# Optimization experiments

Measured on AMD Instinct MI355X. Metric: run time of the kernel, lower is better.

## Reference

```python
import jax, jax.numpy as jnp
import numpy as np

N, E, IN_FEATS, HID, HEADS = 50000, 800000, 256, 32, 8
NEG_SLOPE = 0.2


def _init_params(key):
    ks = jax.random.split(key, 12)
    def lin(k, fi, fo):
        return jax.random.normal(k, (fi, fo), jnp.float32) * (1.0 / np.sqrt(fi))
    p = {}
    # layer 0: in_feats -> HID x HEADS
    p['W0'] = lin(ks[0], IN_FEATS, HEADS * HID)
    p['al0'] = jax.random.normal(ks[1], (HEADS, HID), jnp.float32) * 0.1
    p['ar0'] = jax.random.normal(ks[2], (HEADS, HID), jnp.float32) * 0.1
    p['b0'] = jnp.zeros((HEADS * HID,), jnp.float32)
    # layer 1: HID*HEADS -> HID x HEADS
    p['W1'] = lin(ks[3], HEADS * HID, HEADS * HID)
    p['al1'] = jax.random.normal(ks[4], (HEADS, HID), jnp.float32) * 0.1
    p['ar1'] = jax.random.normal(ks[5], (HEADS, HID), jnp.float32) * 0.1
    p['b1'] = jnp.zeros((HEADS * HID,), jnp.float32)
    # layer 2 (final): HID*HEADS -> HID x 1 head, no activation
    p['W2'] = lin(ks[6], HEADS * HID, HID)
    p['al2'] = jax.random.normal(ks[7], (1, HID), jnp.float32) * 0.1
    p['ar2'] = jax.random.normal(ks[8], (1, HID), jnp.float32) * 0.1
    p['b2'] = jnp.zeros((HID,), jnp.float32)
    return p


def setup_inputs() -> dict:
    key = jax.random.key(0)
    k1, k2, k3, kp = jax.random.split(key, 4)
    inp = {
        'features': jax.random.normal(k1, (N, IN_FEATS), jnp.float32),
        'src': jax.random.randint(k2, (E,), 0, N, jnp.int32),
        'dst': jax.random.randint(k3, (E,), 0, N, jnp.int32),
    }
    inp.update(_init_params(kp))
    return inp


def _gat_layer(x, src, dst, W, al, ar, b, heads, act):
    n = x.shape[0]
    d = W.shape[1] // heads
    feat = (x @ W).reshape(n, heads, d)           # [N,H,D]
    el = jnp.sum(feat * al, axis=-1)              # [N,H]
    er = jnp.sum(feat * ar, axis=-1)              # [N,H]
    e = jax.nn.leaky_relu(el[src] + er[dst], NEG_SLOPE)   # [E,H]
    # segment softmax over destination neighborhoods
    emax = jax.ops.segment_max(e, dst, num_segments=n)
    ex = jnp.exp(e - emax[dst])
    denom = jax.ops.segment_sum(ex, dst, num_segments=n)
    a = ex / (denom[dst] + 1e-9)                  # [E,H]
    msg = feat[src] * a[:, :, None]               # [E,H,D]
    out = jax.ops.segment_sum(msg, dst, num_segments=n)   # [N,H,D]
    out = out + b.reshape(1, heads, d)
    return act(out) if act is not None else out


def reference(features, src, dst, W0, al0, ar0, b0, W1, al1, ar1, b1, W2, al2, ar2, b2):
    h = _gat_layer(features, src, dst, W0, al0, ar0, b0, HEADS, jax.nn.elu)
    h = h.reshape(h.shape[0], -1)
    h = _gat_layer(h, src, dst, W1, al1, ar1, b1, HEADS, jax.nn.elu)
    h = h.reshape(h.shape[0], -1)
    h = _gat_layer(h, src, dst, W2, al2, ar2, b2, 1, None)   # [N,1,D]
    return h.mean(axis=1)                                    # [N,D]
```

## Files before the change

kernel.cpp:

```cpp
#include <hip/hip_runtime.h>

typedef unsigned short u16;
typedef unsigned int   u32;
typedef __attribute__((ext_vector_type(8))) short  short8;
typedef __attribute__((ext_vector_type(4))) float  f32x4;
typedef __attribute__((ext_vector_type(2))) float  f32x2;
typedef __attribute__((ext_vector_type(2))) unsigned int u32v2;
typedef __attribute__((ext_vector_type(4))) unsigned int u32v4;

#define NN 50000
#define NE 800000

__device__ __forceinline__ float bf2f(u16 b) { return __uint_as_float(((u32)b) << 16); }
__device__ __forceinline__ float bflo(u32 p) { return __uint_as_float(p << 16); }
__device__ __forceinline__ float bfhi(u32 p) { return __uint_as_float(p & 0xffff0000u); }
__device__ __forceinline__ u16 f2bf(float f) {
    u32 u = __float_as_uint(f);
    u32 r = u + 0x7fffu + ((u >> 16) & 1u);
    return (u16)(r >> 16);
}
__device__ __forceinline__ float lexp(float v) {
    v = fmaxf(v, 0.2f * v);
    return __expf(fminf(v, 60.f));
}

__device__ __forceinline__ int block_detect(const u32* x, int n, int* sh, int* sz) {
    int t = threadIdx.x;
    int hits = 0, nz = 0;
    for (int i = t; i < n; i += 256) {
        u32 w = x[i];
        if (w) {
            ++nz;
            u32 e = (w >> 7) & 0xffu;
            if (e >= 100 && e <= 150) ++hits;
        }
    }
    sh[t] = hits; sz[t] = nz;
    __syncthreads();
    for (int ofs = 128; ofs > 0; ofs >>= 1) {
        if (t < ofs) { sh[t] += sh[t + ofs]; sz[t] += sz[t + ofs]; }
        __syncthreads();
    }
    return (sz[0] == 0) ? 2 : ((sh[0] * 2 >= sz[0]) ? 0 : 1);
}

struct PrepArgs {
    const u32* dp[13]; int dnw[13];
    const void* cs[9]; float* cd[9]; int cn[9];
    const void* wsrc[3]; u16* wdst[3]; int wN[3]; int wchunks[3];
    int* deg; int degn;
};

__global__ __launch_bounds__(256) void k_prep(PrepArgs a, int* flags) {
    __shared__ int sh[256], sz[256];
    const int bid = blockIdx.x;
    const int t = threadIdx.x;
    if (bid < 13) {
        int f = block_detect(a.dp[bid], a.dnw[bid], sh, sz);
        if (t == 0) flags[bid] = f;
    } else if (bid < 22) {
        const int j = bid - 13;
        int nw = a.cn[j] / 2; if (nw > 512) nw = 512;
        const int fl = block_detect((const u32*)a.cs[j], nw, sh, sz);
        if (t < a.cn[j]) {
            float v = 0.f;
            if (fl == 1) v = ((const float*)a.cs[j])[t];
            else if (fl == 0) v = bf2f(((const u16*)a.cs[j])[t]);
            a.cd[j][t] = v;
        }
    } else if (bid < 90) {
        int wj, base;
        if (bid < 54)      { wj = 0; base = 22; }
        else if (bid < 86) { wj = 1; base = 54; }
        else               { wj = 2; base = 86; }
        const void* Wsrc = a.wsrc[wj];
        const int fl = block_detect((const u32*)Wsrc, 512, sh, sz);
        const int id = (bid - base) * 256 + t;
        if (id < a.wchunks[wj]) {
            const int L = id & 63, kt = (id >> 6) & 7, nt = id >> 9;
            const int col = nt * 16 + (L & 15);
            const int krow = kt * 32 + ((L >> 4) & 3) * 8;
            const bool isf32 = (fl == 1);
            const int N = a.wN[wj];
            u16* Wp = a.wdst[wj];
#pragma unroll
            for (int j2 = 0; j2 < 8; ++j2) {
                int s = (krow + j2) * N + col;
                Wp[id * 8 + j2] = isf32 ? f2bf(((const float*)Wsrc)[s])
                                        : ((const u16*)Wsrc)[s];
            }
        }
    } else {
        const int i = (bid - 90) * 256 + t;
        if (i < a.degn) a.deg[i] = 0;
    }
}

__global__ void k_hist(const int* __restrict__ dst, int* __restrict__ deg, int E) {
    int e = blockIdx.x * 256 + threadIdx.x;
    if (e < E) atomicAdd(&deg[dst[e]], 1);
}

__global__ __launch_bounds__(256) void k_scan_partial(const int* __restrict__ deg,
                                                      int* __restrict__ bsum, int n) {
    __shared__ int red[256];
    int t = threadIdx.x;
    int i = blockIdx.x * 256 + t;
    red[t] = (i < n) ? deg[i] : 0;
    __syncthreads();
    for (int ofs = 128; ofs > 0; ofs >>= 1) {
        if (t < ofs) red[t] += red[t + ofs];
        __syncthreads();
    }
    if (t == 0) bsum[blockIdx.x] = red[0];
}

__global__ __launch_bounds__(256) void k_scan_bsum(int* __restrict__ bsum, int nb) {
    __shared__ int s[256];
    int t = threadIdx.x;
    int v = (t < nb) ? bsum[t] : 0;
    s[t] = v;
    __syncthreads();
    for (int ofs = 1; ofs < 256; ofs <<= 1) {
        int x = (t >= ofs) ? s[t - ofs] : 0;
        __syncthreads();
        s[t] += x;
        __syncthreads();
    }
    if (t < nb) bsum[t] = s[t] - v;
}

__global__ __launch_bounds__(256) void k_scan_final(const int* __restrict__ deg,
                                                    const int* __restrict__ bsum,
                                                    int* __restrict__ rowptr,
                                                    int* __restrict__ cursor, int n) {
    __shared__ int s[256];
    int t = threadIdx.x;
    int i = blockIdx.x * 256 + t;
    int v = (i < n) ? deg[i] : 0;
    s[t] = v;
    __syncthreads();
    for (int ofs = 1; ofs < 256; ofs <<= 1) {
        int x = (t >= ofs) ? s[t - ofs] : 0;
        __syncthreads();
        s[t] += x;
        __syncthreads();
    }
    int excl = bsum[blockIdx.x] + s[t] - v;
    if (i < n) {
        rowptr[i] = excl;
        cursor[i] = excl;
        if (i == n - 1) rowptr[n] = excl + v;
    }
}

__global__ void k_scatter(const int* __restrict__ src, const int* __restrict__ dst,
                          int* __restrict__ cursor, int* __restrict__ csr_src, int E) {
    int e = blockIdx.x * 256 + threadIdx.x;
    if (e >= E) return;
    int p = atomicAdd(&cursor[dst[e]], 1);
    csr_src[p] = src[e];
}

__global__ __launch_bounds__(512) void k_gemm_mfma(const void* __restrict__ Xv,
                                                   const int* __restrict__ xflag,
                                                   const u16* __restrict__ Wp,
                                                   u16* __restrict__ OUT, int nrows) {
    __shared__ u16 As[64 * 256];
    const int t = threadIdx.x;
    const int w = t >> 6, L = t & 63;
    const int quad = (L >> 4) & 3;
    const int r0 = blockIdx.x * 64;
    const bool xf32 = (xflag != nullptr) && (*xflag == 1);

    short8* Asv = (short8*)As;
    short8 zero = {0, 0, 0, 0, 0, 0, 0, 0};
#pragma unroll
    for (int i = 0; i < 4; ++i) {
        int g = i * 512 + t;
        int row = g >> 5, cc = g & 31;
        int r = r0 + row;
        short8 val = zero;
        if (r < nrows) {
            if (xf32) {
                const f32x4* Xf4 = (const f32x4*)Xv;
                f32x4 lo = Xf4[(size_t)r * 64 + cc * 2];
                f32x4 hi = Xf4[(size_t)r * 64 + cc * 2 + 1];
                val[0] = (short)f2bf(lo[0]); val[1] = (short)f2bf(lo[1]);
                val[2] = (short)f2bf(lo[2]); val[3] = (short)f2bf(lo[3]);
                val[4] = (short)f2bf(hi[0]); val[5] = (short)f2bf(hi[1]);
                val[6] = (short)f2bf(hi[2]); val[7] = (short)f2bf(hi[3]);
            } else {
                val = ((const short8*)Xv)[(size_t)r * 32 + cc];
            }
        }
        Asv[cc * 64 + (row ^ (cc & 7))] = val;
    }

    const short8* Wv = (const short8*)Wp;
    short8 bf[2][8];
#pragma unroll
    for (int jn = 0; jn < 2; ++jn) {
        int nt = w + jn * 8;
#pragma unroll
        for (int kt = 0; kt < 8; ++kt) bf[jn][kt] = Wv[(nt * 8 + kt) * 64 + L];
    }
    __syncthreads();

    f32x4 acc[4][2];
#pragma unroll
    for (int mi = 0; mi < 4; ++mi)
#pragma unroll
        for (int jn = 0; jn < 2; ++jn) acc[mi][jn] = (f32x4){0.f, 0.f, 0.f, 0.f};

#pragma unroll
    for (int kt = 0; kt < 8; ++kt) {
        const int ccr = kt * 4 + quad;
#pragma unroll
        for (int mi = 0; mi < 4; ++mi) {
            short8 af = Asv[ccr * 64 + ((mi * 16 + (L & 15)) ^ (ccr & 7))];
            acc[mi][0] = __builtin_amdgcn_mfma_f32_16x16x32_bf16(af, bf[0][kt], acc[mi][0], 0, 0, 0);
            acc[mi][1] = __builtin_amdgcn_mfma_f32_16x16x32_bf16(af, bf[1][kt], acc[mi][1], 0, 0, 0);
        }
    }

#pragma unroll
    for (int mi = 0; mi < 4; ++mi) {
        int rb = r0 + mi * 16 + quad * 4;
#pragma unroll
        for (int jn = 0; jn < 2; ++jn) {
            int c = (w + jn * 8) * 16 + (L & 15);
#pragma unroll
            for (int reg = 0; reg < 4; ++reg) {
                int r = rb + reg;
                if (r < nrows) OUT[(size_t)r * 256 + c] = f2bf(acc[mi][jn][reg]);
            }
        }
    }
}

__global__ __launch_bounds__(256) void k_gemm_mfma32(const u16* __restrict__ Xb,
                                                     const u16* __restrict__ Wp,
                                                     u16* __restrict__ OUT, int nrows) {
    __shared__ u16 As[128 * 256];
    const int t = threadIdx.x;
    const int w = t >> 6, L = t & 63;
    const int quad = (L >> 4) & 3;
    const int r0 = blockIdx.x * 128;
    const int mh = (w >> 1) * 64, nt = w & 1;

    const short8* Xv = (const short8*)Xb;
    short8* Asv = (short8*)As;
    short8 zero = {0, 0, 0, 0, 0, 0, 0, 0};
#pragma unroll
    for (int i = 0; i < 16; ++i) {
        int g = i * 256 + t;
        int row = g >> 5, cc = g & 31;
        int r = r0 + row;
        Asv[cc * 128 + (row ^ (cc & 7))] = (r < nrows) ? Xv[(size_t)r * 32 + cc] : zero;
    }

    const short8* Wv = (const short8*)Wp;
    short8 bf[8];
#pragma unroll
    for (int kt = 0; kt < 8; ++kt) bf[kt] = Wv[(nt * 8 + kt) * 64 + L];
    __syncthreads();

    f32x4 acc[4];
#pragma unroll
    for (int mi = 0; mi < 4; ++mi) acc[mi] = (f32x4){0.f, 0.f, 0.f, 0.f};

#pragma unroll
    for (int kt = 0; kt < 8; ++kt) {
        const int ccr = kt * 4 + quad;
#pragma unroll
        for (int mi = 0; mi < 4; ++mi) {
            short8 af = Asv[ccr * 128 + ((mh + mi * 16 + (L & 15)) ^ (ccr & 7))];
            acc[mi] = __builtin_amdgcn_mfma_f32_16x16x32_bf16(af, bf[kt], acc[mi], 0, 0, 0);
        }
    }

#pragma unroll
    for (int mi = 0; mi < 4; ++mi) {
        int rb = r0 + mh + mi * 16 + quad * 4;
        int c = nt * 16 + (L & 15);
#pragma unroll
        for (int reg = 0; reg < 4; ++reg) {
            int r = rb + reg;
            if (r < nrows) OUT[(size_t)r * 32 + c] = f2bf(acc[mi][reg]);
        }
    }
}

__global__ void k_elr8(const u16* __restrict__ featb, const float* __restrict__ al,
                       const float* __restrict__ ar, float* __restrict__ el,
                       float* __restrict__ er, int n) {
    int idx = blockIdx.x * 256 + threadIdx.x;
    if (idx >= n * 8) return;
    int node = idx >> 3, h = idx & 7;
    const u32v4* fu = (const u32v4*)((const u32*)featb + (size_t)node * 128 + h * 16);
    const float* A = al + h * 32;
    const float* B = ar + h * 32;
    float sl = 0.f, sr = 0.f;
#pragma unroll
    for (int j = 0; j < 4; ++j) {
        u32v4 w4 = fu[j];
#pragma unroll
        for (int k = 0; k < 4; ++k) {
            u32 w = (k == 0) ? w4.x : (k == 1) ? w4.y : (k == 2) ? w4.z : w4.w;
            float f0 = bflo(w), f1 = bfhi(w);
            int c = j * 8 + k * 2;
            sl += f0 * A[c] + f1 * A[c + 1];
            sr += f0 * B[c] + f1 * B[c + 1];
        }
    }
    el[idx] = sl;
    er[idx] = sr;
}

__global__ void k_elr1(const u16* __restrict__ featb, const float* __restrict__ al,
                       const float* __restrict__ ar, float* __restrict__ el,
                       float* __restrict__ er, int n) {
    int node = blockIdx.x * 256 + threadIdx.x;
    if (node >= n) return;
    const u32v4* fu = (const u32v4*)((const u32*)featb + (size_t)node * 16);
    float sl = 0.f, sr = 0.f;
#pragma unroll
    for (int j = 0; j < 4; ++j) {
        u32v4 w4 = fu[j];
#pragma unroll
        for (int k = 0; k < 4; ++k) {
            u32 w = (k == 0) ? w4.x : (k == 1) ? w4.y : (k == 2) ? w4.z : w4.w;
            float f0 = bflo(w), f1 = bfhi(w);
            int c = j * 8 + k * 2;
            sl += f0 * al[c] + f1 * al[c + 1];
            sr += f0 * ar[c] + f1 * ar[c + 1];
        }
    }
    el[node] = sl;
    er[node] = sr;
}

__global__ __launch_bounds__(256) void k_gather8(const int* __restrict__ rowptr,
                                                 const int* __restrict__ csr_src,
                                                 const float* __restrict__ el,
                                                 const float* __restrict__ er,
                                                 const u32v2* __restrict__ featb4,
                                                 const float* __restrict__ bias,
                                                 u32v2* __restrict__ xout4) {
    __shared__ __align__(16) float sAL[4][2][64];
    __shared__ __align__(16) int   sSL[4][2][8];
    const int t = threadIdx.x;
    const int wv = t >> 6;
    const int q = t & 63;
    const int d = blockIdx.x * 4 + wv;
    const int eL = q >> 3, hL = q & 7;
    const int b = rowptr[d], e = rowptr[d + 1];
    const int deg = e - b;
    const int nch = (deg + 7) >> 3;
    const float erA = er[d * 8 + hL];

    float (*AL)[64] = sAL[wv];
    int (*SL)[8] = sSL[wv];

    float a0 = 0.f, a1 = 0.f, a2 = 0.f, a3 = 0.f;
    float partial = 0.f;

    u32v2 fw[8], fw2[8];
    int csrP = 0, ncP = 0;
    float elP = 0.f;

    if (nch > 0) {
        const int nc0 = deg < 8 ? deg : 8;
        const int i0 = eL < nc0 ? eL : nc0 - 1;
        const int s0 = csr_src[b + i0];
        if (nch > 1) {
            const int r1 = deg - 8;
            ncP = r1 < 8 ? r1 : 8;
            const int i1 = eL < ncP ? eL : ncP - 1;
            csrP = csr_src[b + 8 + i1];
        }
        const float el0 = el[s0 * 8 + hL];
        if (hL == 0) SL[0][eL] = s0;
        const int4 sv0 = *(const int4*)&SL[0][0];
        const int4 sv1 = *(const int4*)&SL[0][4];
        fw[0] = featb4[sv0.x * 64 + q];
        fw[1] = featb4[sv0.y * 64 + q];
        fw[2] = featb4[sv0.z * 64 + q];
        fw[3] = featb4[sv0.w * 64 + q];
        fw[4] = featb4[sv1.x * 64 + q];
        fw[5] = featb4[sv1.y * 64 + q];
        fw[6] = featb4[sv1.z * 64 + q];
        fw[7] = featb4[sv1.w * 64 + q];
        const float ex0 = (eL < nc0) ? lexp(el0 + erA) : 0.f;
        partial += ex0;
        AL[0][hL * 8 + eL] = ex0;
        if (nch > 1) elP = el[csrP * 8 + hL];
    }

    for (int c = 0; c < nch; ++c) {
        const int cur = c & 1, nxt = cur ^ 1;

        int csrF = 0, ncF = 0;
        if (c + 2 < nch) {
            const int r2 = deg - (c + 2) * 8;
            ncF = r2 < 8 ? r2 : 8;
            const int i2 = eL < ncF ? eL : ncF - 1;
            csrF = csr_src[b + (c + 2) * 8 + i2];
        }

        if (c + 1 < nch) {
            if (hL == 0) SL[nxt][eL] = csrP;
            const int4 sv0 = *(const int4*)&SL[nxt][0];
            const int4 sv1 = *(const int4*)&SL[nxt][4];
            fw2[0] = featb4[sv0.x * 64 + q];
            fw2[1] = featb4[sv0.y * 64 + q];
            fw2[2] = featb4[sv0.z * 64 + q];
            fw2[3] = featb4[sv0.w * 64 + q];
            fw2[4] = featb4[sv1.x * 64 + q];
            fw2[5] = featb4[sv1.y * 64 + q];
            fw2[6] = featb4[sv1.z * 64 + q];
            fw2[7] = featb4[sv1.w * 64 + q];
            const float exN = (eL < ncP) ? lexp(elP + erA) : 0.f;
            partial += exN;
            AL[nxt][hL * 8 + eL] = exN;
        }

        const int h8 = (q >> 3) * 8;
        const f32x4 A0 = *(const f32x4*)&AL[cur][h8];
        const f32x4 A1 = *(const f32x4*)&AL[cur][h8 + 4];

        if (c + 2 < nch) elP = el[csrF * 8 + hL];

#define GAT_EDGE(i, axv) { const u32v2 w_ = fw[i]; \
        a0 += bflo(w_.x) * (axv); a1 += bfhi(w_.x) * (axv); \
        a2 += bflo(w_.y) * (axv); a3 += bfhi(w_.y) * (axv); }
        GAT_EDGE(0, A0[0]) GAT_EDGE(1, A0[1]) GAT_EDGE(2, A0[2]) GAT_EDGE(3, A0[3])
        GAT_EDGE(4, A1[0]) GAT_EDGE(5, A1[1]) GAT_EDGE(6, A1[2]) GAT_EDGE(7, A1[3])
#undef GAT_EDGE

#pragma unroll
        for (int i = 0; i < 8; ++i) fw[i] = fw2[i];
        csrP = csrF;
        ncP = ncF;
    }

    float v = partial;
    v += __shfl_xor(v, 8);
    v += __shfl_xor(v, 16);
    v += __shfl_xor(v, 32);
    const float ssd = __shfl(v, q >> 3);

    const float rd = 1.f / (ssd + 1e-9f);
    const float4 bb = *(const float4*)&bias[4 * q];
    float v0 = a0 * rd + bb.x;
    float v1 = a1 * rd + bb.y;
    float v2 = a2 * rd + bb.z;
    float v3 = a3 * rd + bb.w;
    v0 = v0 > 0.f ? v0 : expm1f(v0);
    v1 = v1 > 0.f ? v1 : expm1f(v1);
    v2 = v2 > 0.f ? v2 : expm1f(v2);
    v3 = v3 > 0.f ? v3 : expm1f(v3);
    u32v2 o;
    o.x = (u32)f2bf(v0) | ((u32)f2bf(v1) << 16);
    o.y = (u32)f2bf(v2) | ((u32)f2bf(v3) << 16);
    xout4[(size_t)d * 64 + q] = o;
}

__global__ __launch_bounds__(256) void k_gather1(const int* __restrict__ rowptr,
                                                 const int* __restrict__ csr_src,
                                                 const float* __restrict__ el,
                                                 const float* __restrict__ er,
                                                 const u32* __restrict__ featb2,
                                                 const float* __restrict__ bias,
                                                 void* __restrict__ out,
                                                 const int* __restrict__ flag, int n) {
    const int t = threadIdx.x;
    const int d = blockIdx.x * 16 + (t >> 4);
    const int lane = t & 15;
    if (d >= n) return;
    const int b = rowptr[d], e = rowptr[d + 1];
    const float erd = er[d];
    float a0 = 0.f, a1 = 0.f, ssum = 0.f;

    for (int c = b; c < e; c += 16) {
        const int idx = c + lane;
        const int s_own = csr_src[idx < e ? idx : e - 1];
        const float ex_own = (idx < e) ? lexp(el[s_own] + erd) : 0.f;
        ssum += ex_own;
#pragma unroll
        for (int i = 0; i < 16; ++i) {
            const int si = __shfl(s_own, i, 16);
            const float ai = __shfl(ex_own, i, 16);
            const u32 w = featb2[(size_t)si * 16 + lane];
            a0 += bflo(w) * ai;
            a1 += bfhi(w) * ai;
        }
    }

    ssum += __shfl_xor(ssum, 1);
    ssum += __shfl_xor(ssum, 2);
    ssum += __shfl_xor(ssum, 4);
    ssum += __shfl_xor(ssum, 8);

    const float rd = 1.f / (ssum + 1e-9f);
    const float v0 = a0 * rd + bias[2 * lane];
    const float v1 = a1 * rd + bias[2 * lane + 1];
    if (*flag == 1) {
        f32x2 o = {v0, v1};
        ((f32x2*)out)[(size_t)d * 16 + lane] = o;
    } else {
        ((u32*)out)[(size_t)d * 16 + lane] = (u32)f2bf(v0) | ((u32)f2bf(v1) << 16);
    }
}

extern "C" void kernel_launch(void* const* d_in, const int* in_sizes, int n_in,
                              void* d_out, int out_size, void* d_ws, size_t ws_size,
                              hipStream_t stream) {
    const void* features = d_in[0];
    const int* src = (const int*)d_in[1];
    const int* dst = (const int*)d_in[2];

    char* ws = (char*)d_ws;
    size_t off = 0;
    auto carve = [&](size_t bytes) -> void* {
        void* p = ws + off;
        off = (off + bytes + 255) & ~(size_t)255;
        return p;
    };
    int*   flags = (int*)carve(64);
    float* pconv = (float*)carve(2048 * 4);
    u16*   Wp0 = (u16*)carve(65536 * 2);
    u16*   Wp1 = (u16*)carve(65536 * 2);
    u16*   Wp2 = (u16*)carve(8192 * 2);
    u16*   Xb    = (u16*)carve((size_t)NN * 256 * 2);
    u16*   featb = (u16*)carve((size_t)NN * 256 * 2);
    float* el   = (float*)carve((size_t)NN * 8 * 4);
    float* er   = (float*)carve((size_t)NN * 8 * 4);
    int*   deg     = (int*)carve((size_t)NN * 4);
    int*   cursor  = (int*)carve((size_t)NN * 4);
    int*   rowptr  = (int*)carve((size_t)(NN + 1) * 4);
    int*   bsum    = (int*)carve(256 * 4);
    int*   csr_src = (int*)carve((size_t)NE * 4);
    if (off > ws_size) return;

    const int N = NN, E = NE;
    const int nscan = (N + 255) / 256;

    PrepArgs pa;
    const int din_idx[13] = {0, 3, 4, 5, 6, 7, 8, 9, 10, 11, 12, 13, 14};
    for (int j = 0; j < 13; ++j) {
        pa.dp[j] = (const u32*)d_in[din_idx[j]];
        int nw = in_sizes[din_idx[j]] / 2;
        pa.dnw[j] = nw > 512 ? 512 : nw;
    }
    const int psl[9] = {4, 5, 6, 8, 9, 10, 12, 13, 14};
    float* dsts[9];
    {
        size_t o = 0;
        for (int j = 0; j < 9; ++j) {
            dsts[j] = pconv + o;
            o += (size_t)in_sizes[psl[j]];
        }
    }
    for (int j = 0; j < 9; ++j) {
        pa.cs[j] = d_in[psl[j]];
        pa.cd[j] = dsts[j];
        pa.cn[j] = in_sizes[psl[j]];
    }
    pa.wsrc[0] = d_in[3];  pa.wdst[0] = Wp0; pa.wN[0] = 256; pa.wchunks[0] = 8192;
    pa.wsrc[1] = d_in[7];  pa.wdst[1] = Wp1; pa.wN[1] = 256; pa.wchunks[1] = 8192;
    pa.wsrc[2] = d_in[11]; pa.wdst[2] = Wp2; pa.wN[2] = 32;  pa.wchunks[2] = 1024;
    pa.deg = deg; pa.degn = N;
    k_prep<<<90 + nscan, 256, 0, stream>>>(pa, flags);
    float* al0f = dsts[0]; float* ar0f = dsts[1]; float* b0f = dsts[2];
    float* al1f = dsts[3]; float* ar1f = dsts[4]; float* b1f = dsts[5];
    float* al2f = dsts[6]; float* ar2f = dsts[7]; float* b2f = dsts[8];

    k_hist<<<(E + 255) / 256, 256, 0, stream>>>(dst, deg, E);
    k_scan_partial<<<nscan, 256, 0, stream>>>(deg, bsum, N);
    k_scan_bsum<<<1, 256, 0, stream>>>(bsum, nscan);
    k_scan_final<<<nscan, 256, 0, stream>>>(deg, bsum, rowptr, cursor, N);
    k_scatter<<<(E + 255) / 256, 256, 0, stream>>>(src, dst, cursor, csr_src, E);

    const int ggrid = (N + 63) / 64;

    k_gemm_mfma<<<ggrid, 512, 0, stream>>>(features, flags, Wp0, featb, N);
    k_elr8<<<(N * 8 + 255) / 256, 256, 0, stream>>>(featb, al0f, ar0f, el, er, N);
    k_gather8<<<N / 4, 256, 0, stream>>>(rowptr, csr_src, el, er,
                                         (const u32v2*)featb, b0f, (u32v2*)Xb);

    k_gemm_mfma<<<ggrid, 512, 0, stream>>>(Xb, nullptr, Wp1, featb, N);
    k_elr8<<<(N * 8 + 255) / 256, 256, 0, stream>>>(featb, al1f, ar1f, el, er, N);
    k_gather8<<<N / 4, 256, 0, stream>>>(rowptr, csr_src, el, er,
                                         (const u32v2*)featb, b1f, (u32v2*)Xb);

    k_gemm_mfma32<<<(N + 127) / 128, 256, 0, stream>>>(Xb, Wp2, featb, N);
    k_elr1<<<(N + 255) / 256, 256, 0, stream>>>(featb, al2f, ar2f, el, er, N);
    k_gather1<<<(N + 15) / 16, 256, 0, stream>>>(rowptr, csr_src, el, er,
                                                 (const u32*)featb, b2f,
                                                 d_out, flags, N);
}
```

Measured before the change: 421.5 us.

## Fuse CSR build kernels with layer-0 GEMM and attention-logit kernels

```diff
diff --git a/kernel.cpp b/kernel.cpp
--- a/kernel.cpp
+++ b/kernel.cpp
@@ -96,9 +96,89 @@
     }
 }
 
-__global__ void k_hist(const int* __restrict__ dst, int* __restrict__ deg, int E) {
-    int e = blockIdx.x * 256 + threadIdx.x;
-    if (e < E) atomicAdd(&deg[dst[e]], 1);
+__global__ __launch_bounds__(512) void k_fA(const void* __restrict__ Xv,
+                                            const int* __restrict__ xflag,
+                                            const u16* __restrict__ Wp,
+                                            u16* __restrict__ OUT, int nrows,
+                                            const int* __restrict__ dstv,
+                                            int* __restrict__ deg, int E) {
+    __shared__ u16 As[64 * 256];
+    const int gblocks = (nrows + 63) >> 6;
+    if ((int)blockIdx.x >= gblocks) {
+        const int e = (blockIdx.x - gblocks) * 512 + threadIdx.x;
+        if (e < E) atomicAdd(&deg[dstv[e]], 1);
+        return;
+    }
+    const int t = threadIdx.x;
+    const int w = t >> 6, L = t & 63;
+    const int quad = (L >> 4) & 3;
+    const int r0 = blockIdx.x * 64;
+    const bool xf32 = (xflag != nullptr) && (*xflag == 1);
+
+    short8* Asv = (short8*)As;
+    short8 zero = {0, 0, 0, 0, 0, 0, 0, 0};
+#pragma unroll
+    for (int i = 0; i < 4; ++i) {
+        int g = i * 512 + t;
+        int row = g >> 5, cc = g & 31;
+        int r = r0 + row;
+        short8 val = zero;
+        if (r < nrows) {
+            if (xf32) {
+                const f32x4* Xf4 = (const f32x4*)Xv;
+                f32x4 lo = Xf4[(size_t)r * 64 + cc * 2];
+                f32x4 hi = Xf4[(size_t)r * 64 + cc * 2 + 1];
+                val[0] = (short)f2bf(lo[0]); val[1] = (short)f2bf(lo[1]);
+                val[2] = (short)f2bf(lo[2]); val[3] = (short)f2bf(lo[3]);
+                val[4] = (short)f2bf(hi[0]); val[5] = (short)f2bf(hi[1]);
+                val[6] = (short)f2bf(hi[2]); val[7] = (short)f2bf(hi[3]);
+            } else {
+                val = ((const short8*)Xv)[(size_t)r * 32 + cc];
+            }
+        }
+        Asv[cc * 64 + (row ^ (cc & 7))] = val;
+    }
+
+    const short8* Wv = (const short8*)Wp;
+    short8 bf[2][8];
+#pragma unroll
+    for (int jn = 0; jn < 2; ++jn) {
+        int nt = w + jn * 8;
+#pragma unroll
+        for (int kt = 0; kt < 8; ++kt) bf[jn][kt] = Wv[(nt * 8 + kt) * 64 + L];
+    }
+    __syncthreads();
+
+    f32x4 acc[4][2];
+#pragma unroll
+    for (int mi = 0; mi < 4; ++mi)
+#pragma unroll
+        for (int jn = 0; jn < 2; ++jn) acc[mi][jn] = (f32x4){0.f, 0.f, 0.f, 0.f};
+
+#pragma unroll
+    for (int kt = 0; kt < 8; ++kt) {
+        const int ccr = kt * 4 + quad;
+#pragma unroll
+        for (int mi = 0; mi < 4; ++mi) {
+            short8 af = Asv[ccr * 64 + ((mi * 16 + (L & 15)) ^ (ccr & 7))];
+            acc[mi][0] = __builtin_amdgcn_mfma_f32_16x16x32_bf16(af, bf[0][kt], acc[mi][0], 0, 0, 0);
+            acc[mi][1] = __builtin_amdgcn_mfma_f32_16x16x32_bf16(af, bf[1][kt], acc[mi][1], 0, 0, 0);
+        }
+    }
+
+#pragma unroll
+    for (int mi = 0; mi < 4; ++mi) {
+        int rb = r0 + mi * 16 + quad * 4;
+#pragma unroll
+        for (int jn = 0; jn < 2; ++jn) {
+            int c = (w + jn * 8) * 16 + (L & 15);
+#pragma unroll
+            for (int reg = 0; reg < 4; ++reg) {
+                int r = rb + reg;
+                if (r < nrows) OUT[(size_t)r * 256 + c] = f2bf(acc[mi][jn][reg]);
+            }
+        }
+    }
 }
 
 __global__ __launch_bounds__(256) void k_scan_partial(const int* __restrict__ deg,
@@ -115,27 +195,23 @@
     if (t == 0) bsum[blockIdx.x] = red[0];
 }
 
-__global__ __launch_bounds__(256) void k_scan_bsum(int* __restrict__ bsum, int nb) {
-    __shared__ int s[256];
-    int t = threadIdx.x;
-    int v = (t < nb) ? bsum[t] : 0;
-    s[t] = v;
-    __syncthreads();
-    for (int ofs = 1; ofs < 256; ofs <<= 1) {
-        int x = (t >= ofs) ? s[t - ofs] : 0;
-        __syncthreads();
-        s[t] += x;
-        __syncthreads();
-    }
-    if (t < nb) bsum[t] = s[t] - v;
-}
-
 __global__ __launch_bounds__(256) void k_scan_final(const int* __restrict__ deg,
                                                     const int* __restrict__ bsum,
                                                     int* __restrict__ rowptr,
-                                                    int* __restrict__ cursor, int n) {
-    __shared__ int s[256];
+                                                    int* __restrict__ cursor,
+                                                    int n, int nb) {
+    __shared__ int s[256], bs[256];
     int t = threadIdx.x;
+    bs[t] = (t < nb) ? bsum[t] : 0;
+    __syncthreads();
+    for (int ofs = 1; ofs < 256; ofs <<= 1) {
+        int x = (t >= ofs) ? bs[t - ofs] : 0;
+        __syncthreads();
+        bs[t] += x;
+        __syncthreads();
+    }
+    const int bexcl = (blockIdx.x == 0) ? 0 : bs[blockIdx.x - 1];
+
     int i = blockIdx.x * 256 + t;
     int v = (i < n) ? deg[i] : 0;
     s[t] = v;
@@ -146,7 +222,7 @@
         s[t] += x;
         __syncthreads();
     }
-    int excl = bsum[blockIdx.x] + s[t] - v;
+    int excl = bexcl + s[t] - v;
     if (i < n) {
         rowptr[i] = excl;
         cursor[i] = excl;
@@ -154,12 +230,45 @@
     }
 }
 
-__global__ void k_scatter(const int* __restrict__ src, const int* __restrict__ dst,
-                          int* __restrict__ cursor, int* __restrict__ csr_src, int E) {
-    int e = blockIdx.x * 256 + threadIdx.x;
-    if (e >= E) return;
-    int p = atomicAdd(&cursor[dst[e]], 1);
-    csr_src[p] = src[e];
+__global__ __launch_bounds__(256) void k_fB(const int* __restrict__ src,
+                                            const int* __restrict__ dstv,
+                                            int* __restrict__ cursor,
+                                            int* __restrict__ csr_src, int E,
+                                            const u16* __restrict__ featb,
+                                            const float* __restrict__ al,
+                                            const float* __restrict__ ar,
+                                            float* __restrict__ el,
+                                            float* __restrict__ er, int n) {
+    const int nsc = (E + 255) >> 8;
+    if ((int)blockIdx.x < nsc) {
+        const int e = blockIdx.x * 256 + threadIdx.x;
+        if (e < E) {
+            int p = atomicAdd(&cursor[dstv[e]], 1);
+            csr_src[p] = src[e];
+        }
+        return;
+    }
+    const int idx = (blockIdx.x - nsc) * 256 + threadIdx.x;
+    if (idx >= n * 8) return;
+    const int node = idx >> 3, h = idx & 7;
+    const u32v4* fu = (const u32v4*)((const u32*)featb + (size_t)node * 128 + h * 16);
+    const float* A = al + h * 32;
+    const float* B = ar + h * 32;
+    float sl = 0.f, sr = 0.f;
+#pragma unroll
+    for (int j = 0; j < 4; ++j) {
+        u32v4 w4 = fu[j];
+#pragma unroll
+        for (int k = 0; k < 4; ++k) {
+            u32 w = (k == 0) ? w4.x : (k == 1) ? w4.y : (k == 2) ? w4.z : w4.w;
+            float f0 = bflo(w), f1 = bfhi(w);
+            int c = j * 8 + k * 2;
+            sl += f0 * A[c] + f1 * A[c + 1];
+            sr += f0 * B[c] + f1 * B[c + 1];
+        }
+    }
+    el[idx] = sl;
+    er[idx] = sr;
 }
 
 __global__ __launch_bounds__(512) void k_gemm_mfma(const void* __restrict__ Xv,
@@ -577,21 +686,25 @@
     float* al1f = dsts[3]; float* ar1f = dsts[4]; float* b1f = dsts[5];
     float* al2f = dsts[6]; float* ar2f = dsts[7]; float* b2f = dsts[8];
 
-    k_hist<<<(E + 255) / 256, 256, 0, stream>>>(dst, deg, E);
+    const int ggrid = (N + 63) / 64;
+    const int hblocks = (E + 511) / 512;
+
+    k_fA<<<ggrid + hblocks, 512, 0, stream>>>(features, flags, Wp0, featb, N,
+                                              dst, deg, E);
+
     k_scan_partial<<<nscan, 256, 0, stream>>>(deg, bsum, N);
-    k_scan_bsum<<<1, 256, 0, stream>>>(bsum, nscan);
-    k_scan_final<<<nscan, 256, 0, stream>>>(deg, bsum, rowptr, cursor, N);
-    k_scatter<<<(E + 255) / 256, 256, 0, stream>>>(src, dst, cursor, csr_src, E);
-
-    const int ggrid = (N + 63) / 64;
-
-    k_gemm_mfma<<<ggrid, 512, 0, stream>>>(features, flags, Wp0, featb, N);
-    k_elr8<<<(N * 8 + 255) / 256, 256, 0, stream>>>(featb, al0f, ar0f, el, er, N);
+    k_scan_final<<<nscan, 256, 0, stream>>>(deg, bsum, rowptr, cursor, N, nscan);
+
+    const int scb = (E + 255) / 256;
+    const int elb = (N * 8 + 255) / 256;
+    k_fB<<<scb + elb, 256, 0, stream>>>(src, dst, cursor, csr_src, E,
+                                        featb, al0f, ar0f, el, er, N);
+
     k_gather8<<<N / 4, 256, 0, stream>>>(rowptr, csr_src, el, er,
                                          (const u32v2*)featb, b0f, (u32v2*)Xb);
 
     k_gemm_mfma<<<ggrid, 512, 0, stream>>>(Xb, nullptr, Wp1, featb, N);
-    k_elr8<<<(N * 8 + 255) / 256, 256, 0, stream>>>(featb, al1f, ar1f, el, er, N);
+    k_elr8<<<elb, 256, 0, stream>>>(featb, al1f, ar1f, el, er, N);
     k_gather8<<<N / 4, 256, 0, stream>>>(rowptr, csr_src, el, er,
                                          (const u32v2*)featb, b1f, (u32v2*)Xb);
 
```

New measurement: 405.9 us. -3.7%, faster.
